# Kernel tuning notes

Measured on AMD Instinct MI355X. Metric: run time of the kernel, lower is better.

The kernel has to match this reference:

```python
import jax, jax.numpy as jnp
import numpy as np
import math

B, S, D, H = 2, 2048, 1024, 16
HD = D // H  # head_dim = 64


def setup_inputs() -> dict:
    key = jax.random.key(0)
    k1, k2, k3, k4, k5 = jax.random.split(key, 5)
    scale_in = 1.0 / math.sqrt(D)
    return {
        "x": jax.random.normal(k1, (B, S, D), dtype=jnp.float32),
        "Wqkv": jax.random.normal(k2, (3 * D, D), dtype=jnp.float32) * scale_in,
        "bqkv": jax.random.normal(k3, (3 * D,), dtype=jnp.float32) * 0.01,
        "Wout": jax.random.normal(k4, (D, D), dtype=jnp.float32) * scale_in,
        "bout": jax.random.normal(k5, (D,), dtype=jnp.float32) * 0.01,
    }


def reference(x, Wqkv, bqkv, Wout, bout):
    Bs, Sl, Dm = x.shape
    # qkv projection: torch Linear is x @ W.T + b
    qkv = x @ Wqkv.T + bqkv                        # [B,S,3D]
    qkv = qkv.reshape(Bs, Sl, 3, H, HD)
    q, k, v = qkv[:, :, 0], qkv[:, :, 1], qkv[:, :, 2]  # each [B,S,H,d]
    softmax_scale = 1.0 / math.sqrt(HD)
    # NOTE: source einsum 'bshd,btjd->bsht' sums k over its head axis j.
    # Equivalent efficient form: pre-sum k (and v) over heads.
    k_sum = k.sum(axis=2)                          # [B,S,d]
    v_sum = v.sum(axis=2)                          # [B,S,d]
    scores = jnp.einsum('bshd,btd->bsht', q, k_sum) * softmax_scale  # [B,S,H,T]
    causal_mask = jnp.triu(jnp.ones((Sl, Sl), dtype=bool), k=1)      # [S,T]
    scores = jnp.where(causal_mask[None, :, None, :], -jnp.inf, scores)
    attn = jax.nn.softmax(scores, axis=-1)
    # dropout p=0.0 / eval mode -> identity
    out = jnp.einsum('bsht,btd->bshd', attn, v_sum)  # [B,S,H,d]
    out = out.reshape(Bs, Sl, Dm)
    return out @ Wout.T + bout
```

## Files before the change

kernel.cpp:

```cpp
#include <hip/hip_runtime.h>


#define S_LEN 2048
#define DIM 1024

using floatx4 = __attribute__((ext_vector_type(4))) float;
using halfx8  = __attribute__((ext_vector_type(8))) _Float16;
using halfx4  = __attribute__((ext_vector_type(4))) _Float16;

__device__ __forceinline__ floatx4 mfma16(halfx8 a, halfx8 b, floatx4 c) {
  return __builtin_amdgcn_mfma_f32_16x16x32_f16(a, b, c, 0, 0, 0);
}

__device__ __forceinline__ void gll16(const void* g, void* l) {
  __builtin_amdgcn_global_load_lds(
      (const __attribute__((address_space(1))) void*)g,
      (__attribute__((address_space(3))) void*)l, 16, 0, 0);
}

__global__ __launch_bounds__(256) void prep_all(
    const float* __restrict__ x, const float* __restrict__ wqkv,
    const float* __restrict__ bqkv, const float* __restrict__ wout,
    _Float16* __restrict__ xb, _Float16* __restrict__ wcomb,
    _Float16* __restrict__ woutb, float* __restrict__ bcomb) {
  int bx = blockIdx.x;
  if (bx < 6144) {
    size_t i4 = ((size_t)bx * 256 + threadIdx.x) * 4;
    const float* src;
    _Float16* dst;
    size_t off;
    if (i4 < 4194304) { src = x; dst = xb; off = i4; }
    else if (i4 < 5242880) { src = wqkv; dst = wcomb; off = i4 - 4194304; }
    else { src = wout; dst = woutb; off = i4 - 5242880; }
    float4 v = *(const float4*)(src + off);
    halfx4 o;
    o[0] = (_Float16)v.x; o[1] = (_Float16)v.y;
    o[2] = (_Float16)v.z; o[3] = (_Float16)v.w;
    *(halfx4*)(dst + off) = o;
  } else {
    int gid = (bx - 6144) * 256 + threadIdx.x;
    int c = gid >> 10, j = gid & 1023;
    int row0 = (c < 64) ? (1024 + c) : (2048 + c - 64);
    float s = 0.f;
#pragma unroll
    for (int h = 0; h < 16; ++h) s += wqkv[(size_t)(row0 + h * 64) * 1024 + j];
    wcomb[(size_t)1024 * 1024 + gid] = (_Float16)s;
    if (gid < 1024) bcomb[gid] = bqkv[gid];
    if (gid < 128) {
      int b0 = (gid < 64) ? (1024 + gid) : (2048 + gid - 64);
      float sb = 0.f;
#pragma unroll
      for (int h = 0; h < 16; ++h) sb += bqkv[b0 + h * 64];
      bcomb[1024 + gid] = sb;
    }
  }
}

template <int MODE>
__global__ __launch_bounds__(256, 3) void gemm_t4(
    const _Float16* __restrict__ A, const _Float16* __restrict__ W,
    const float* __restrict__ bias, void* __restrict__ Cv,
    _Float16* __restrict__ kbo, _Float16* __restrict__ vto) {
  const int K = 1024;
  __shared__ _Float16 As[64][64];
  __shared__ _Float16 Ws[128][64];
  int tid = threadIdx.x;
  int lane = tid & 63, w = tid >> 6, ln = lane & 15, q4 = lane >> 4;
  int m0 = blockIdx.x * 64, n0 = blockIdx.y * 128;
  int rr = lane >> 3, gg = ((lane & 7) ^ rr) * 8;
  const _Float16* agp = A + (size_t)(m0 + w * 16 + rr) * K + gg;
  const _Float16* wgp = W + (size_t)(n0 + w * 32 + rr) * K + gg;
  floatx4 acc[4][2] = {};
  for (int kt = 0; kt < K; kt += 64) {
    __syncthreads();
#pragma unroll
    for (int j = 0; j < 2; ++j)
      gll16(agp + (size_t)(8 * j) * K + kt, &As[w * 16 + 8 * j][0]);
#pragma unroll
    for (int j = 0; j < 4; ++j)
      gll16(wgp + (size_t)(8 * j) * K + kt, &Ws[w * 32 + 8 * j][0]);
    __syncthreads();
#pragma unroll
    for (int kh = 0; kh < 2; ++kh) {
      int sw = ((q4 + 4 * kh) ^ (ln & 7)) * 8;
      halfx8 bf[2];
#pragma unroll
      for (int nf = 0; nf < 2; ++nf)
        bf[nf] = *(const halfx8*)&Ws[w * 32 + nf * 16 + ln][sw];
#pragma unroll
      for (int mf = 0; mf < 4; ++mf) {
        halfx8 af = *(const halfx8*)&As[mf * 16 + ln][sw];
#pragma unroll
        for (int nf = 0; nf < 2; ++nf)
          acc[mf][nf] = mfma16(af, bf[nf], acc[mf][nf]);
      }
    }
  }
  const float qscale = 0.18033688011112042f;
#pragma unroll
  for (int nf = 0; nf < 2; ++nf) {
    int col = n0 + w * 32 + nf * 16 + ln;
    float bv = bias[col];
    if constexpr (MODE == 1) {
#pragma unroll
      for (int mf = 0; mf < 4; ++mf)
#pragma unroll
        for (int i = 0; i < 4; ++i) {
          int row = m0 + mf * 16 + q4 * 4 + i;
          ((float*)Cv)[(size_t)row * 1024 + col] = acc[mf][nf][i] + bv;
        }
    } else {
      if (col < 1024) {
#pragma unroll
        for (int mf = 0; mf < 4; ++mf)
#pragma unroll
          for (int i = 0; i < 4; ++i) {
            int row = m0 + mf * 16 + q4 * 4 + i;
            ((_Float16*)Cv)[(size_t)row * 1024 + col] =
                (_Float16)((acc[mf][nf][i] + bv) * qscale);
          }
      } else if (col < 1088) {
        int ck = col - 1024;
#pragma unroll
        for (int mf = 0; mf < 4; ++mf)
#pragma unroll
          for (int i = 0; i < 4; ++i) {
            int row = m0 + mf * 16 + q4 * 4 + i;
            kbo[(size_t)row * 64 + ck] = (_Float16)(acc[mf][nf][i] + bv);
          }
      } else {
        int d = col - 1088;
#pragma unroll
        for (int mf = 0; mf < 4; ++mf) {
          int row0 = m0 + mf * 16 + q4 * 4;
          int bb = row0 >> 11, sps = row0 & 2047;
          halfx4 o;
#pragma unroll
          for (int i = 0; i < 4; ++i) o[i] = (_Float16)(acc[mf][nf][i] + bv);
          *(halfx4*)&vto[((size_t)((bb << 6) + d)) * S_LEN + sps] = o;
        }
      }
    }
  }
}

__global__ __launch_bounds__(512, 4) void flash_attn12(
    const _Float16* __restrict__ Qb, const _Float16* __restrict__ kb,
    const _Float16* __restrict__ vtb, _Float16* __restrict__ aob) {
  __shared__ _Float16 Ks[128][64];
  __shared__ _Float16 Vt[64][128];
  __shared__ _Float16 Ps[8][2048];
  int tid = threadIdx.x;
  int lane = tid & 63, w = tid >> 6, ln = lane & 15, q4 = lane >> 4;
  int bx = (int)blockIdx.x;
  int lo = bx & 255;
  int b = lo & 1;
  int crow = (bx >> 8) ? (255 - (lo >> 1)) : (lo >> 1);
  int s0 = crow * 8;
  int s = s0 + w;
  size_t bS = (size_t)b * S_LEN;

  int rr = lane >> 3, ggk = ((lane & 7) ^ rr) * 8;
  const _Float16* kgp = kb + (bS + w * 16 + rr) * 64 + ggk;
  int vr = lane >> 4;
  int vhalf = (lane >> 3) & 1, vg = lane & 7;
  const _Float16* vgp[2];
#pragma unroll
  for (int j = 0; j < 2; ++j) {
    int row = w * 8 + 4 * j + vr;
    vgp[j] = vtb + ((size_t)b * 64 + row) * S_LEN + vhalf * 64 +
             ((vg ^ (row & 7)) * 8);
  }
  int swk0 = (q4 ^ (ln & 7)) * 8;
  int swk1 = ((q4 + 4) ^ (ln & 7)) * 8;
  _Float16* Pw = &Ps[w][0];
  int pwbase = (q4 >> 1) * 128 + ln * 8 + (q4 & 1) * 4;
  int prbase = q4 * 128 + ln * 8;

  const _Float16* qp = Qb + (bS + s) * DIM + ln * 64 + q4 * 8;
  halfx8 bq0 = *(const halfx8*)qp, bq1 = *(const halfx8*)(qp + 32);

  float m_run = -1e30f, l_run = 0.f;
  floatx4 oacc[4] = {};
  int nt = (crow >> 4) + 1;

  for (int it = 0; it < nt; ++it) {
    int t0 = it << 7;
    __syncthreads();
    gll16(kgp + (size_t)t0 * 64, &Ks[w * 16][0]);
    gll16(kgp + (size_t)(t0 + 8) * 64, &Ks[w * 16 + 8][0]);
    gll16(vgp[0] + t0, &Vt[w * 8][0]);
    gll16(vgp[1] + t0, &Vt[w * 8 + 4][0]);
    __syncthreads();

    floatx4 sf[2][4];
    __builtin_amdgcn_s_setprio(1);
#pragma unroll
    for (int tq = 0; tq < 2; ++tq)
#pragma unroll
      for (int tf = 0; tf < 4; ++tf) {
        halfx8 ak0 = *(const halfx8*)&Ks[tq * 64 + tf * 16 + ln][swk0];
        halfx8 ak1 = *(const halfx8*)&Ks[tq * 64 + tf * 16 + ln][swk1];
        floatx4 z = {};
        z = mfma16(ak0, bq0, z);
        sf[tq][tf] = mfma16(ak1, bq1, z);
      }
    __builtin_amdgcn_s_setprio(0);
    if (it == nt - 1) {
#pragma unroll
      for (int tq = 0; tq < 2; ++tq)
#pragma unroll
        for (int tf = 0; tf < 4; ++tf)
#pragma unroll
          for (int i = 0; i < 4; ++i) {
            int t = t0 + tq * 64 + tf * 16 + q4 * 4 + i;
            if (t > s) sf[tq][tf][i] = -1e30f;
          }
    }
    float tm = -1e30f;
#pragma unroll
    for (int tq = 0; tq < 2; ++tq)
#pragma unroll
      for (int tf = 0; tf < 4; ++tf)
        tm = fmaxf(tm, fmaxf(fmaxf(sf[tq][tf][0], sf[tq][tf][1]),
                             fmaxf(sf[tq][tf][2], sf[tq][tf][3])));
    tm = fmaxf(tm, __shfl_xor(tm, 16));
    tm = fmaxf(tm, __shfl_xor(tm, 32));
    if (!__all(tm <= m_run + 8.f)) {
      float mn = fmaxf(m_run, tm);
      float alpha = exp2f(m_run - mn);
      m_run = mn;
      l_run *= alpha;
#pragma unroll
      for (int n2 = 0; n2 < 4; ++n2)
#pragma unroll
        for (int i = 0; i < 4; ++i) oacc[n2][i] *= alpha;
    }
    float rs = 0.f;
#pragma unroll
    for (int tq = 0; tq < 2; ++tq)
#pragma unroll
      for (int tf = 0; tf < 4; ++tf) {
        float p0 = exp2f(sf[tq][tf][0] - m_run);
        float p1 = exp2f(sf[tq][tf][1] - m_run);
        float p2 = exp2f(sf[tq][tf][2] - m_run);
        float p3 = exp2f(sf[tq][tf][3] - m_run);
        rs += (p0 + p1) + (p2 + p3);
        halfx4 pk;
        pk[0] = (_Float16)p0; pk[1] = (_Float16)p1;
        pk[2] = (_Float16)p2; pk[3] = (_Float16)p3;
        *(halfx4*)&Pw[(tq * 8 + tf * 2) * 128 + pwbase] = pk;
      }
    rs += __shfl_xor(rs, 16);
    rs += __shfl_xor(rs, 32);
    l_run += rs;
    halfx8 bp[4];
#pragma unroll
    for (int kc = 0; kc < 4; ++kc)
      bp[kc] = *(const halfx8*)&Pw[kc * 512 + prbase];
    __builtin_amdgcn_s_setprio(1);
#pragma unroll
    for (int kc = 0; kc < 4; ++kc) {
      int half = (kc >> 1) * 64;
      int sw = ((q4 + 4 * (kc & 1)) ^ (ln & 7)) * 8;
#pragma unroll
      for (int n2 = 0; n2 < 4; ++n2) {
        halfx8 av = *(const halfx8*)&Vt[n2 * 16 + ln][half + sw];
        oacc[n2] = mfma16(av, bp[kc], oacc[n2]);
      }
    }
    __builtin_amdgcn_s_setprio(0);
  }
  float inv = 1.0f / l_run;
#pragma unroll
  for (int n2 = 0; n2 < 4; ++n2) {
    halfx4 o;
#pragma unroll
    for (int i = 0; i < 4; ++i) o[i] = (_Float16)(oacc[n2][i] * inv);
    *(halfx4*)(aob + (bS + s) * DIM + ln * 64 + n2 * 16 + q4 * 4) = o;
  }
}

extern "C" void kernel_launch(void* const* d_in, const int* in_sizes, int n_in,
                              void* d_out, int out_size, void* d_ws,
                              size_t ws_size, hipStream_t stream) {
  const float* x    = (const float*)d_in[0];
  const float* wqkv = (const float*)d_in[1];
  const float* bqkv = (const float*)d_in[2];
  const float* wout = (const float*)d_in[3];
  const float* bout = (const float*)d_in[4];
  float* out = (float*)d_out;
  char* ws = (char*)d_ws;
  _Float16* xb    = (_Float16*)(ws);
  _Float16* qb    = (_Float16*)(ws + (8u << 20));
  _Float16* aob   = (_Float16*)(ws + (16u << 20));
  _Float16* kb    = (_Float16*)(ws + (24u << 20));
  _Float16* vtb   = (_Float16*)(ws + (24u << 20) + (512u << 10));
  _Float16* wcomb = (_Float16*)(ws + (25u << 20));
  _Float16* woutb = (_Float16*)(ws + (27u << 20) + (512u << 10));
  float*    bcomb = (float*)(ws + (29u << 20) + (512u << 10));

  hipLaunchKernelGGL(prep_all, dim3(6656), dim3(256), 0, stream,
                     x, wqkv, bqkv, wout, xb, wcomb, woutb, bcomb);
  hipLaunchKernelGGL((gemm_t4<0>), dim3(64, 9), dim3(256), 0, stream,
                     xb, wcomb, bcomb, (void*)qb, kb, vtb);
  hipLaunchKernelGGL(flash_attn12, dim3(512), dim3(512), 0, stream,
                     qb, kb, vtb, aob);
  hipLaunchKernelGGL((gemm_t4<1>), dim3(64, 8), dim3(256), 0, stream,
                     aob, woutb, bout, (void*)out, nullptr, nullptr);
}
```

Before: 165.9 us.

## Permute V-transpose layout so softmax P stays in registers, drop LDS staging

The QKV GEMM epilogue now writes the transposed V in a permuted order within each 128-token block. That order matches the register layout of the score MFMA output. The attention kernel can then pack P directly into fp16 register operands with cvt_pkrtz instead of writing P to shared memory and reading it back. This removes the 32KB Ps LDS buffer and one LDS round trip per tile, which may also raise occupancy. In exchange, V stores become scattered 2-element writes, and P is rounded toward zero rather than to nearest.

```diff
diff --git a/kernel.cpp b/kernel.cpp
--- a/kernel.cpp
+++ b/kernel.cpp
@@ -7,6 +7,8 @@
 using floatx4 = __attribute__((ext_vector_type(4))) float;
 using halfx8  = __attribute__((ext_vector_type(8))) _Float16;
 using halfx4  = __attribute__((ext_vector_type(4))) _Float16;
+using halfx2  = __attribute__((ext_vector_type(2))) _Float16;
+using fp16x2  = __attribute__((ext_vector_type(2))) __fp16;
 
 __device__ __forceinline__ floatx4 mfma16(halfx8 a, halfx8 b, floatx4 c) {
   return __builtin_amdgcn_mfma_f32_16x16x32_f16(a, b, c, 0, 0, 0);
@@ -134,22 +136,28 @@
         for (int mf = 0; mf < 4; ++mf) {
           int row0 = m0 + mf * 16 + q4 * 4;
           int bb = row0 >> 11, sps = row0 & 2047;
-          halfx4 o;
-#pragma unroll
-          for (int i = 0; i < 4; ++i) o[i] = (_Float16)(acc[mf][nf][i] + bv);
-          *(halfx4*)&vto[((size_t)((bb << 6) + d)) * S_LEN + sps] = o;
+          int blk = sps & ~127, tl = sps & 127;
+          int p0 = (tl >> 6) * 64 + ((tl >> 2) & 3) * 8 + ((tl >> 4) & 3) * 2;
+          _Float16* basep =
+              &vto[((size_t)((bb << 6) + d)) * S_LEN + blk];
+          halfx2 lo, hi;
+          lo[0] = (_Float16)(acc[mf][nf][0] + bv);
+          lo[1] = (_Float16)(acc[mf][nf][1] + bv);
+          hi[0] = (_Float16)(acc[mf][nf][2] + bv);
+          hi[1] = (_Float16)(acc[mf][nf][3] + bv);
+          *(halfx2*)&basep[p0] = lo;
+          *(halfx2*)&basep[p0 + 32] = hi;
         }
       }
     }
   }
 }
 
-__global__ __launch_bounds__(512, 4) void flash_attn12(
+__global__ __launch_bounds__(512, 4) void flash_attn13(
     const _Float16* __restrict__ Qb, const _Float16* __restrict__ kb,
     const _Float16* __restrict__ vtb, _Float16* __restrict__ aob) {
   __shared__ _Float16 Ks[128][64];
   __shared__ _Float16 Vt[64][128];
-  __shared__ _Float16 Ps[8][2048];
   int tid = threadIdx.x;
   int lane = tid & 63, w = tid >> 6, ln = lane & 15, q4 = lane >> 4;
   int bx = (int)blockIdx.x;
@@ -173,9 +181,6 @@
   }
   int swk0 = (q4 ^ (ln & 7)) * 8;
   int swk1 = ((q4 + 4) ^ (ln & 7)) * 8;
-  _Float16* Pw = &Ps[w][0];
-  int pwbase = (q4 >> 1) * 128 + ln * 8 + (q4 & 1) * 4;
-  int prbase = q4 * 128 + ln * 8;
 
   const _Float16* qp = Qb + (bS + s) * DIM + ln * 64 + q4 * 8;
   halfx8 bq0 = *(const halfx8*)qp, bq1 = *(const halfx8*)(qp + 32);
@@ -237,6 +242,7 @@
         for (int i = 0; i < 4; ++i) oacc[n2][i] *= alpha;
     }
     float rs = 0.f;
+    unsigned bpw[4][4];
 #pragma unroll
     for (int tq = 0; tq < 2; ++tq)
 #pragma unroll
@@ -246,27 +252,27 @@
         float p2 = exp2f(sf[tq][tf][2] - m_run);
         float p3 = exp2f(sf[tq][tf][3] - m_run);
         rs += (p0 + p1) + (p2 + p3);
-        halfx4 pk;
-        pk[0] = (_Float16)p0; pk[1] = (_Float16)p1;
-        pk[2] = (_Float16)p2; pk[3] = (_Float16)p3;
-        *(halfx4*)&Pw[(tq * 8 + tf * 2) * 128 + pwbase] = pk;
+        union { fp16x2 h; unsigned u; } c0, c1;
+        c0.h = __builtin_amdgcn_cvt_pkrtz(p0, p1);
+        c1.h = __builtin_amdgcn_cvt_pkrtz(p2, p3);
+        bpw[2 * tq][tf] = c0.u;
+        bpw[2 * tq + 1][tf] = c1.u;
       }
     rs += __shfl_xor(rs, 16);
     rs += __shfl_xor(rs, 32);
     l_run += rs;
-    halfx8 bp[4];
-#pragma unroll
-    for (int kc = 0; kc < 4; ++kc)
-      bp[kc] = *(const halfx8*)&Pw[kc * 512 + prbase];
     __builtin_amdgcn_s_setprio(1);
 #pragma unroll
     for (int kc = 0; kc < 4; ++kc) {
+      union { unsigned u[4]; halfx8 v; } bpu;
+#pragma unroll
+      for (int ww = 0; ww < 4; ++ww) bpu.u[ww] = bpw[kc][ww];
       int half = (kc >> 1) * 64;
       int sw = ((q4 + 4 * (kc & 1)) ^ (ln & 7)) * 8;
 #pragma unroll
       for (int n2 = 0; n2 < 4; ++n2) {
         halfx8 av = *(const halfx8*)&Vt[n2 * 16 + ln][half + sw];
-        oacc[n2] = mfma16(av, bp[kc], oacc[n2]);
+        oacc[n2] = mfma16(av, bpu.v, oacc[n2]);
       }
     }
     __builtin_amdgcn_s_setprio(0);
@@ -304,7 +310,7 @@
                      x, wqkv, bqkv, wout, xb, wcomb, woutb, bcomb);
   hipLaunchKernelGGL((gemm_t4<0>), dim3(64, 9), dim3(256), 0, stream,
                      xb, wcomb, bcomb, (void*)qb, kb, vtb);
-  hipLaunchKernelGGL(flash_attn12, dim3(512), dim3(512), 0, stream,
+  hipLaunchKernelGGL(flash_attn13, dim3(512), dim3(512), 0, stream,
                      qb, kb, vtb, aob);
   hipLaunchKernelGGL((gemm_t4<1>), dim3(64, 8), dim3(256), 0, stream,
                      aob, woutb, bout, (void*)out, nullptr, nullptr);
```

Result: no change. 165.9 us (-0.0%).
